# Kernel tuning notes

Measured on AMD Instinct MI355X. Metric: run time of the kernel, lower is better.

The kernel has to match this reference:

```python
import jax, jax.numpy as jnp
import numpy as np

B, CIN, COUT, H, W = 4, 256, 256, 96, 96
GN_GROUPS = 16
EPS = 1e-5


def setup_inputs() -> dict:
    key = jax.random.key(0)
    k0, k1, k2, k3 = jax.random.split(key, 4)
    x = jax.random.normal(k0, (B, CIN, H, W), jnp.float32)
    offset = jax.random.normal(k1, (B, 18, H, W), jnp.float32)
    mask = jax.random.uniform(k2, (B, 9, H, W), jnp.float32)  # modulation scalars (sigmoid-range)
    weight = jax.random.normal(k3, (COUT, CIN, 3, 3), jnp.float32) * 0.02
    gamma = jnp.ones((COUT,), jnp.float32)
    beta = jnp.zeros((COUT,), jnp.float32)
    return {"x": x, "offset": offset, "mask": mask, "weight": weight, "gamma": gamma, "beta": beta}


def _bilinear(xf, py, px, Hs, Ws):
    # xf: [B, C, H*W] flattened input; py/px: [B, H, W] sample coords -> [B, C, H, W]
    y0 = jnp.floor(py)
    x0 = jnp.floor(px)
    acc = jnp.zeros((xf.shape[0], xf.shape[1], py.shape[1], py.shape[2]), xf.dtype)
    for dy in (0, 1):
        for dx in (0, 1):
            yy = y0 + dy
            xx = x0 + dx
            wgt = (1.0 - jnp.abs(py - yy)) * (1.0 - jnp.abs(px - xx))
            valid = (yy >= 0) & (yy < Hs) & (xx >= 0) & (xx < Ws)  # zero-pad outside
            yi = jnp.clip(yy, 0, Hs - 1).astype(jnp.int32)
            xi = jnp.clip(xx, 0, Ws - 1).astype(jnp.int32)
            idx = (yi * Ws + xi).reshape(py.shape[0], -1)  # [B, H*W]
            g = jax.vmap(lambda xb, ib: xb[:, ib])(xf, idx)  # [B, C, H*W]
            g = g.reshape(acc.shape)
            acc = acc + g * (wgt * valid.astype(xf.dtype))[:, None]
    return acc


def _modulated_deform_conv(x, offset, mask, weight):
    # 3x3, stride=1, pad=1, dilation=1, deform_groups=1, no bias
    Bz, C, Hs, Ws = x.shape
    hh = jnp.arange(Hs, dtype=x.dtype)
    ww = jnp.arange(Ws, dtype=x.dtype)
    base_y, base_x = jnp.meshgrid(hh, ww, indexing="ij")  # [H, W]
    xf = x.reshape(Bz, C, Hs * Ws)
    out = jnp.zeros((Bz, weight.shape[0], Hs, Ws), x.dtype)
    for k in range(9):  # fixed 3x3 kernel taps
        ki, kj = k // 3, k % 3
        py = base_y[None] + (ki - 1) + offset[:, 2 * k]      # dy channel
        px = base_x[None] + (kj - 1) + offset[:, 2 * k + 1]  # dx channel
        val = _bilinear(xf, py, px, Hs, Ws) * mask[:, k][:, None]  # [B, CIN, H, W]
        out = out + jnp.einsum("oc,bchw->bohw", weight[:, :, ki, kj], val)
    return out


def _group_norm(x, gamma, beta):
    Bz, C, Hs, Ws = x.shape
    xr = x.reshape(Bz, GN_GROUPS, C // GN_GROUPS, Hs, Ws)
    mu = xr.mean(axis=(2, 3, 4), keepdims=True)
    var = xr.var(axis=(2, 3, 4), keepdims=True)
    xn = ((xr - mu) * jax.lax.rsqrt(var + EPS)).reshape(Bz, C, Hs, Ws)
    return xn * gamma[None, :, None, None] + beta[None, :, None, None]


def reference(x, offset, mask, weight, gamma, beta):
    y = _modulated_deform_conv(x, offset, mask, weight)
    return _group_norm(y, gamma, beta)
```

## Files before the change

### kernel.cpp

```cpp
#include <hip/hip_runtime.h>
#include <hip/hip_bf16.h>
#include <cstdint>

typedef short  short8  __attribute__((ext_vector_type(8)));
typedef ushort ushort8 __attribute__((ext_vector_type(8)));
typedef float  f32x4   __attribute__((ext_vector_type(4)));

#define BATCH 4
#define CIN   256
#define COUT  256
#define HH    96
#define WW    96
#define HWSZ  9216
#define GN_G  16
#define EPSV  1e-5f
#define BN    144
#define NPB   64
#define NWG   (BATCH*NPB)

__device__ __forceinline__ float bf2f(ushort u) {
    return __uint_as_float(((uint32_t)u) << 16);
}
__device__ __forceinline__ ushort f2bf(float f) {
    uint32_t u = __float_as_uint(f);
    u += 0x7FFFu + ((u >> 16) & 1u);
    return (ushort)(u >> 16);
}

__global__ __launch_bounds__(256)
void nhwc_kernel(const float* __restrict__ x, ushort* __restrict__ xn) {
    __shared__ ushort tile[64][66];
    const int b  = blockIdx.z;
    const int cb = blockIdx.y * 64;
    const int pb = blockIdx.x * 64;
    const int t  = threadIdx.x;
    {
        const int pl = t & 63;
        const int cq = t >> 6;
        #pragma unroll
        for (int i = 0; i < 16; ++i) {
            const int c = cq * 16 + i;
            tile[c][pl] = f2bf(x[((size_t)b * CIN + cb + c) * HWSZ + pb + pl]);
        }
    }
    __syncthreads();
    {
        const int cl = t & 63;
        const int pq = t >> 6;
        #pragma unroll
        for (int i = 0; i < 16; ++i) {
            const int p = pq * 16 + i;
            xn[((size_t)b * HWSZ + pb + p) * CIN + cb + cl] = tile[cl][p];
        }
    }
}

__global__ __launch_bounds__(256)
void repack_w_kernel(const float* __restrict__ w, ushort* __restrict__ wp) {
    const int d    = blockIdx.x * 256 + threadIdx.x;
    const int j    = d & 7;
    const int cout = (d >> 3) & 255;
    const int kb8  = d >> 11;
    const int ktap = kb8 >> 5;
    const int cin  = ((kb8 & 31) << 3) | j;
    wp[d] = f2bf(w[cout * (CIN * 9) + cin * 9 + ktap]);
}

__global__ __launch_bounds__(512, 2)
void dcn_mfma_kernel(const ushort* __restrict__ xn, const float* __restrict__ off,
                     const float* __restrict__ msk, const ushort* __restrict__ wp,
                     float* __restrict__ out, float* __restrict__ part) {
    __shared__ __align__(16) ushort buf[2][BN * 128];
    __shared__ int    s_idx[2][BN][4];
    __shared__ float  s_wgt[2][BN][4];

    const int bid  = blockIdx.x;
    const int swz  = (bid & 7) * (NWG / 8) + (bid >> 3);
    const int b    = swz / NPB;
    const int pblk = swz - b * NPB;
    const int p0   = pblk * BN;

    const int t    = threadIdx.x;
    const int lane = t & 63;
    const int wid  = t >> 6;
    const int cg   = wid & 3;
    const int kh   = wid >> 2;

    auto coords = [&](int k) {
        if (t < BN) {
            const int slot = k & 1;
            const int pos  = p0 + t;
            const int hh   = pos / WW;
            const int ww   = pos - hh * WW;
            const size_t obase = ((size_t)b * 18 + 2 * k) * HWSZ + pos;
            const float oy = off[obase];
            const float ox = off[obase + HWSZ];
            const float m  = msk[((size_t)b * 9 + k) * HWSZ + pos];
            const float py = (float)(hh + k / 3 - 1) + oy;
            const float px = (float)(ww + k % 3 - 1) + ox;
            const float y0 = floorf(py), x0 = floorf(px);
            #pragma unroll
            for (int dy = 0; dy < 2; ++dy)
                #pragma unroll
                for (int dx = 0; dx < 2; ++dx) {
                    const float yy = y0 + (float)dy, xx = x0 + (float)dx;
                    const float wb = (1.f - fabsf(py - yy)) * (1.f - fabsf(px - xx));
                    const bool valid = (yy >= 0.f) && (yy < (float)HH) && (xx >= 0.f) && (xx < (float)WW);
                    int yi = (int)yy; yi = yi < 0 ? 0 : (yi > HH - 1 ? HH - 1 : yi);
                    int xi = (int)xx; xi = xi < 0 ? 0 : (xi > WW - 1 ? WW - 1 : xi);
                    s_idx[slot][t][dy * 2 + dx] = yi * WW + xi;
                    s_wgt[slot][t][dy * 2 + dx] = valid ? wb * m : 0.f;
                }
        }
    };

    const int sp  = lane >> 4;
    const int c16 = lane & 15;
    auto stage = [&](int c, ushort* dstbuf) {
        const int tap  = c >> 1;
        const int half = c & 1;
        const int slot = tap & 1;
        const ushort* xb = xn + (size_t)b * HWSZ * CIN + half * 128 + c16 * 8;
        #pragma unroll
        for (int g = 0; g < 5; ++g) {
            const bool active = (g < 4) || (sp < 2);
            const int p = wid * 18 + ((g < 4) ? (g * 4 + sp) : (16 + sp));
            if (active) {
                float vacc[8] = {0.f, 0.f, 0.f, 0.f, 0.f, 0.f, 0.f, 0.f};
                #pragma unroll
                for (int cr = 0; cr < 4; ++cr) {
                    const int   ix = s_idx[slot][p][cr];
                    const float w  = s_wgt[slot][p][cr];
                    const ushort8 v = *(const ushort8*)(xb + (size_t)ix * CIN);
                    #pragma unroll
                    for (int j = 0; j < 8; ++j)
                        vacc[j] += w * bf2f(v[j]);
                }
                ushort8 o;
                #pragma unroll
                for (int j = 0; j < 8; j += 2) {
                    const __hip_bfloat162 h2 = __float22bfloat162_rn(float2{vacc[j], vacc[j + 1]});
                    const uint32_t u = *reinterpret_cast<const uint32_t*>(&h2);
                    o[j]     = (ushort)u;
                    o[j + 1] = (ushort)(u >> 16);
                }
                char* drow = (char*)dstbuf + p * 256;
                *(ushort8*)(drow + ((c16 * 16) ^ ((p & 15) << 4))) = o;
            }
        }
    };

    f32x4 acc[4][9];
    #pragma unroll
    for (int i = 0; i < 4; ++i)
        #pragma unroll
        for (int j = 0; j < 9; ++j)
            acc[i][j] = (f32x4){0.f, 0.f, 0.f, 0.f};

    const int arow = lane & 15;
    const int akb  = lane >> 4;

    auto loadA = [&](int kb8base, int ks, short8 af[4]) {
        const ushort* wrow = wp + ((size_t)(kb8base + ks * 4 + akb) * COUT + cg * 64 + arow) * 8;
        #pragma unroll
        for (int mt = 0; mt < 4; ++mt)
            af[mt] = *(const short8*)(wrow + mt * 16 * 8);
    };

    auto mfma_chunk = [&](int kb8base, const ushort* src, short8 afA[4]) {
        const char* srow = (const char*)src;
        short8 afB[4];
        #pragma unroll
        for (int ks = 0; ks < 2; ++ks) {
            const int ksg = kh * 2 + ks;
            if (ks == 0) loadA(kb8base, kh * 2 + 1, afB);
            short8* afc = ks ? afB : afA;
            #pragma unroll
            for (int nt = 0; nt < 9; ++nt) {
                const int row = arow + nt * 16;
                const short8 bfr = *(const short8*)(srow + row * 256 + ((ksg * 64 + akb * 16) ^ ((row & 15) << 4)));
                #pragma unroll
                for (int mt = 0; mt < 4; ++mt)
                    acc[mt][nt] = __builtin_amdgcn_mfma_f32_16x16x32_bf16(
                        afc[mt], bfr, acc[mt][nt], 0, 0, 0);
            }
        }
    };

    coords(0);
    __syncthreads();
    stage(0, buf[0]);
    __syncthreads();
    for (int c = 0; c < 18; ++c) {
        if (c < 17) stage(c + 1, buf[(c + 1) & 1]);
        if (!(c & 1) && (c >> 1) + 1 < 9) coords((c >> 1) + 1);
        short8 afA[4];
        loadA(c * 16, kh * 2, afA);
        mfma_chunk(c * 16, buf[c & 1], afA);
        __syncthreads();
    }

    {
        f32x4* s_xch = reinterpret_cast<f32x4*>(&buf[0][0]);
        const int plane = cg * 64 + lane;
        #pragma unroll
        for (int mt = 0; mt < 4; ++mt) {
            if (wid >= 4) {
                #pragma unroll
                for (int nt = 0; nt < 9; ++nt)
                    s_xch[plane * 10 + nt] = acc[mt][nt];
            }
            __syncthreads();
            if (wid < 4) {
                #pragma unroll
                for (int nt = 0; nt < 9; ++nt)
                    acc[mt][nt] += s_xch[plane * 10 + nt];
            }
            __syncthreads();
        }
    }

    if (wid < 4) {
        const int prow = lane & 15;
        const int crow = (lane >> 4) * 4;
        #pragma unroll
        for (int mt = 0; mt < 4; ++mt) {
            const int cout = cg * 64 + mt * 16 + crow;
            #pragma unroll
            for (int nt = 0; nt < 9; ++nt) {
                const int opos = p0 + nt * 16 + prow;
                float* op = out + ((size_t)b * COUT + cout) * HWSZ + opos;
                #pragma unroll
                for (int r = 0; r < 4; ++r)
                    op[(size_t)r * HWSZ] = acc[mt][nt][r];
            }
        }

        #pragma unroll
        for (int mt = 0; mt < 4; ++mt) {
            float s = 0.f, q = 0.f;
            #pragma unroll
            for (int nt = 0; nt < 9; ++nt)
                #pragma unroll
                for (int r = 0; r < 4; ++r) {
                    const float v = acc[mt][nt][r];
                    s += v; q += v * v;
                }
            #pragma unroll
            for (int o = 32; o > 0; o >>= 1) {
                s += __shfl_xor(s, o);
                q += __shfl_xor(q, o);
            }
            if (lane == 0) {
                const int bg = b * GN_G + cg * 4 + mt;
                part[((size_t)bg * NPB + pblk) * 2]     = s;
                part[((size_t)bg * NPB + pblk) * 2 + 1] = q;
            }
        }
    }
}

__global__ void gn_final_kernel(const float* __restrict__ part, float* __restrict__ stats) {
    const int t  = threadIdx.x;
    const int bg = t >> 2;
    const int j  = t & 3;
    float s = 0.f, q = 0.f;
    for (int i = j; i < NPB; i += 4) {
        s += part[((size_t)bg * NPB + i) * 2];
        q += part[((size_t)bg * NPB + i) * 2 + 1];
    }
    s += __shfl_xor(s, 1); q += __shfl_xor(q, 1);
    s += __shfl_xor(s, 2); q += __shfl_xor(q, 2);
    if (j == 0) {
        const float invn = 1.f / (float)((COUT / GN_G) * HWSZ);
        const float mean = s * invn;
        stats[bg * 2]     = mean;
        stats[bg * 2 + 1] = q * invn - mean * mean;
    }
}

__global__ __launch_bounds__(256)
void gn_apply_kernel(float* __restrict__ y, const float* __restrict__ stats,
                     const float* __restrict__ gamma, const float* __restrict__ beta) {
    const int i = blockIdx.x * 256 + threadIdx.x;
    const int e = i * 4;
    const int c  = (e / HWSZ) & (COUT - 1);
    const int bg = e / (HWSZ * (COUT / GN_G));
    const float mean = stats[bg * 2];
    const float var  = stats[bg * 2 + 1];
    const float inv  = rsqrtf(var + EPSV);
    const float sc = inv * gamma[c];
    const float sh = beta[c] - mean * sc;
    float4 v = ((float4*)y)[i];
    v.x = v.x * sc + sh;
    v.y = v.y * sc + sh;
    v.z = v.z * sc + sh;
    v.w = v.w * sc + sh;
    ((float4*)y)[i] = v;
}

extern "C" void kernel_launch(void* const* d_in, const int* in_sizes, int n_in,
                              void* d_out, int out_size, void* d_ws, size_t ws_size,
                              hipStream_t stream) {
    const float* x      = (const float*)d_in[0];
    const float* offset = (const float*)d_in[1];
    const float* mask   = (const float*)d_in[2];
    const float* weight = (const float*)d_in[3];
    const float* gamma  = (const float*)d_in[4];
    const float* beta   = (const float*)d_in[5];
    float* out = (float*)d_out;

    ushort* xn    = (ushort*)d_ws;
    ushort* wp    = xn + (size_t)BATCH * HWSZ * CIN;
    float*  part  = (float*)(wp + (size_t)9 * CIN * COUT);
    float*  stats = part + (size_t)BATCH * GN_G * NPB * 2;

    {
        dim3 g(HWSZ / 64, CIN / 64, BATCH);
        nhwc_kernel<<<g, 256, 0, stream>>>(x, xn);
    }
    repack_w_kernel<<<9 * CIN * COUT / 256, 256, 0, stream>>>(weight, wp);

    dcn_mfma_kernel<<<NWG, 512, 0, stream>>>(xn, offset, mask, wp, out, part);

    gn_final_kernel<<<1, 256, 0, stream>>>(part, stats);
    gn_apply_kernel<<<(size_t)BATCH * COUT * HWSZ / 4 / 256, 256, 0, stream>>>(out, stats, gamma, beta);
}
```

Baseline: 105.0 us.

## Use fp16 gather math, bf16 intermediate output, and fuse GN stats into apply

Stores the NHWC input as fp16 and does the bilinear gather blend with packed half-precision vector math instead of per-element fp32 accumulation. When the workspace is large enough, the conv writes its pre-norm output as bf16 to a scratch buffer, and the GroupNorm apply kernel reads that and writes fp32, roughly halving intermediate traffic. The separate GN statistics kernel is folded into the apply kernel, with each block reducing its group's partial sums, which removes one launch. This adds fp16 range and rounding risk in the sampling step and bf16 rounding of the pre-norm activations.

```diff
diff --git a/kernel.cpp b/kernel.cpp
--- a/kernel.cpp
+++ b/kernel.cpp
@@ -2,9 +2,10 @@
 #include <hip/hip_bf16.h>
 #include <cstdint>
 
-typedef short  short8  __attribute__((ext_vector_type(8)));
-typedef ushort ushort8 __attribute__((ext_vector_type(8)));
-typedef float  f32x4   __attribute__((ext_vector_type(4)));
+typedef short    short8  __attribute__((ext_vector_type(8)));
+typedef ushort   ushort8 __attribute__((ext_vector_type(8)));
+typedef float    f32x4   __attribute__((ext_vector_type(4)));
+typedef _Float16 half8   __attribute__((ext_vector_type(8)));
 
 #define BATCH 4
 #define CIN   256
@@ -28,8 +29,8 @@
 }
 
 __global__ __launch_bounds__(256)
-void nhwc_kernel(const float* __restrict__ x, ushort* __restrict__ xn) {
-    __shared__ ushort tile[64][66];
+void nhwc_kernel(const float* __restrict__ x, _Float16* __restrict__ xn) {
+    __shared__ _Float16 tile[64][66];
     const int b  = blockIdx.z;
     const int cb = blockIdx.y * 64;
     const int pb = blockIdx.x * 64;
@@ -40,7 +41,7 @@
         #pragma unroll
         for (int i = 0; i < 16; ++i) {
             const int c = cq * 16 + i;
-            tile[c][pl] = f2bf(x[((size_t)b * CIN + cb + c) * HWSZ + pb + pl]);
+            tile[c][pl] = (_Float16)x[((size_t)b * CIN + cb + c) * HWSZ + pb + pl];
         }
     }
     __syncthreads();
@@ -67,9 +68,10 @@
 }
 
 __global__ __launch_bounds__(512, 2)
-void dcn_mfma_kernel(const ushort* __restrict__ xn, const float* __restrict__ off,
+void dcn_mfma_kernel(const _Float16* __restrict__ xn, const float* __restrict__ off,
                      const float* __restrict__ msk, const ushort* __restrict__ wp,
-                     float* __restrict__ out, float* __restrict__ part) {
+                     float* __restrict__ out, ushort* __restrict__ yb, int use_bf16,
+                     float* __restrict__ part) {
     __shared__ __align__(16) ushort buf[2][BN * 128];
     __shared__ int    s_idx[2][BN][4];
     __shared__ float  s_wgt[2][BN][4];
@@ -83,7 +85,7 @@
     const int t    = threadIdx.x;
     const int lane = t & 63;
     const int wid  = t >> 6;
-    const int cg   = wid & 3;
+    const int cgp  = wid & 3;
     const int kh   = wid >> 2;
 
     auto coords = [&](int k) {
@@ -120,26 +122,26 @@
         const int tap  = c >> 1;
         const int half = c & 1;
         const int slot = tap & 1;
-        const ushort* xb = xn + (size_t)b * HWSZ * CIN + half * 128 + c16 * 8;
+        const _Float16* xb = xn + (size_t)b * HWSZ * CIN + half * 128 + c16 * 8;
         #pragma unroll
         for (int g = 0; g < 5; ++g) {
             const bool active = (g < 4) || (sp < 2);
             const int p = wid * 18 + ((g < 4) ? (g * 4 + sp) : (16 + sp));
             if (active) {
-                float vacc[8] = {0.f, 0.f, 0.f, 0.f, 0.f, 0.f, 0.f, 0.f};
-                #pragma unroll
-                for (int cr = 0; cr < 4; ++cr) {
-                    const int   ix = s_idx[slot][p][cr];
-                    const float w  = s_wgt[slot][p][cr];
-                    const ushort8 v = *(const ushort8*)(xb + (size_t)ix * CIN);
-                    #pragma unroll
-                    for (int j = 0; j < 8; ++j)
-                        vacc[j] += w * bf2f(v[j]);
-                }
+                const _Float16 w0 = (_Float16)s_wgt[slot][p][0];
+                const _Float16 w1 = (_Float16)s_wgt[slot][p][1];
+                const _Float16 w2 = (_Float16)s_wgt[slot][p][2];
+                const _Float16 w3 = (_Float16)s_wgt[slot][p][3];
+                const half8 v0 = *(const half8*)(xb + (size_t)s_idx[slot][p][0] * CIN);
+                const half8 v1 = *(const half8*)(xb + (size_t)s_idx[slot][p][1] * CIN);
+                const half8 v2 = *(const half8*)(xb + (size_t)s_idx[slot][p][2] * CIN);
+                const half8 v3 = *(const half8*)(xb + (size_t)s_idx[slot][p][3] * CIN);
+                const half8 h = v0 * w0 + v1 * w1 + v2 * w2 + v3 * w3;
                 ushort8 o;
                 #pragma unroll
                 for (int j = 0; j < 8; j += 2) {
-                    const __hip_bfloat162 h2 = __float22bfloat162_rn(float2{vacc[j], vacc[j + 1]});
+                    const __hip_bfloat162 h2 =
+                        __float22bfloat162_rn(float2{(float)h[j], (float)h[j + 1]});
                     const uint32_t u = *reinterpret_cast<const uint32_t*>(&h2);
                     o[j]     = (ushort)u;
                     o[j + 1] = (ushort)(u >> 16);
@@ -161,7 +163,7 @@
     const int akb  = lane >> 4;
 
     auto loadA = [&](int kb8base, int ks, short8 af[4]) {
-        const ushort* wrow = wp + ((size_t)(kb8base + ks * 4 + akb) * COUT + cg * 64 + arow) * 8;
+        const ushort* wrow = wp + ((size_t)(kb8base + ks * 4 + akb) * COUT + cgp * 64 + arow) * 8;
         #pragma unroll
         for (int mt = 0; mt < 4; ++mt)
             af[mt] = *(const short8*)(wrow + mt * 16 * 8);
@@ -202,7 +204,7 @@
 
     {
         f32x4* s_xch = reinterpret_cast<f32x4*>(&buf[0][0]);
-        const int plane = cg * 64 + lane;
+        const int plane = cgp * 64 + lane;
         #pragma unroll
         for (int mt = 0; mt < 4; ++mt) {
             if (wid >= 4) {
@@ -223,16 +225,31 @@
     if (wid < 4) {
         const int prow = lane & 15;
         const int crow = (lane >> 4) * 4;
-        #pragma unroll
-        for (int mt = 0; mt < 4; ++mt) {
-            const int cout = cg * 64 + mt * 16 + crow;
-            #pragma unroll
-            for (int nt = 0; nt < 9; ++nt) {
-                const int opos = p0 + nt * 16 + prow;
-                float* op = out + ((size_t)b * COUT + cout) * HWSZ + opos;
-                #pragma unroll
-                for (int r = 0; r < 4; ++r)
-                    op[(size_t)r * HWSZ] = acc[mt][nt][r];
+        if (use_bf16) {
+            #pragma unroll
+            for (int mt = 0; mt < 4; ++mt) {
+                const int cout = cgp * 64 + mt * 16 + crow;
+                #pragma unroll
+                for (int nt = 0; nt < 9; ++nt) {
+                    const int opos = p0 + nt * 16 + prow;
+                    ushort* op = yb + ((size_t)b * COUT + cout) * HWSZ + opos;
+                    #pragma unroll
+                    for (int r = 0; r < 4; ++r)
+                        op[(size_t)r * HWSZ] = f2bf(acc[mt][nt][r]);
+                }
+            }
+        } else {
+            #pragma unroll
+            for (int mt = 0; mt < 4; ++mt) {
+                const int cout = cgp * 64 + mt * 16 + crow;
+                #pragma unroll
+                for (int nt = 0; nt < 9; ++nt) {
+                    const int opos = p0 + nt * 16 + prow;
+                    float* op = out + ((size_t)b * COUT + cout) * HWSZ + opos;
+                    #pragma unroll
+                    for (int r = 0; r < 4; ++r)
+                        op[(size_t)r * HWSZ] = acc[mt][nt][r];
+                }
             }
         }
 
@@ -252,7 +269,7 @@
                 q += __shfl_xor(q, o);
             }
             if (lane == 0) {
-                const int bg = b * GN_G + cg * 4 + mt;
+                const int bg = b * GN_G + cgp * 4 + mt;
                 part[((size_t)bg * NPB + pblk) * 2]     = s;
                 part[((size_t)bg * NPB + pblk) * 2 + 1] = q;
             }
@@ -260,43 +277,85 @@
     }
 }
 
-__global__ void gn_final_kernel(const float* __restrict__ part, float* __restrict__ stats) {
+__global__ __launch_bounds__(256)
+void gn_apply_bf16_kernel(const ushort* __restrict__ yb, const float* __restrict__ part,
+                          const float* __restrict__ gamma, const float* __restrict__ beta,
+                          float* __restrict__ out) {
+    __shared__ float sm[2];
+    const int bg = blockIdx.y;
     const int t  = threadIdx.x;
-    const int bg = t >> 2;
-    const int j  = t & 3;
-    float s = 0.f, q = 0.f;
-    for (int i = j; i < NPB; i += 4) {
-        s += part[((size_t)bg * NPB + i) * 2];
-        q += part[((size_t)bg * NPB + i) * 2 + 1];
-    }
-    s += __shfl_xor(s, 1); q += __shfl_xor(q, 1);
-    s += __shfl_xor(s, 2); q += __shfl_xor(q, 2);
-    if (j == 0) {
-        const float invn = 1.f / (float)((COUT / GN_G) * HWSZ);
-        const float mean = s * invn;
-        stats[bg * 2]     = mean;
-        stats[bg * 2 + 1] = q * invn - mean * mean;
+    if (t < 64) {
+        float s = part[((size_t)bg * NPB + t) * 2];
+        float q = part[((size_t)bg * NPB + t) * 2 + 1];
+        #pragma unroll
+        for (int o = 32; o > 0; o >>= 1) {
+            s += __shfl_xor(s, o);
+            q += __shfl_xor(q, o);
+        }
+        if (t == 0) {
+            const float invn = 1.f / (float)((COUT / GN_G) * HWSZ);
+            const float mean = s * invn;
+            const float var  = q * invn - mean * mean;
+            sm[0] = mean;
+            sm[1] = rsqrtf(var + EPSV);
+        }
+    }
+    __syncthreads();
+    const float mean = sm[0], inv = sm[1];
+    const size_t base = (size_t)bg * (COUT / GN_G) * HWSZ + (size_t)blockIdx.x * 16384;
+    #pragma unroll 2
+    for (int it = 0; it < 8; ++it) {
+        const size_t e = base + ((size_t)(it * 256 + t)) * 8;
+        const int c = (int)((e / HWSZ) & (COUT - 1));
+        const float sc = inv * gamma[c];
+        const float sh = beta[c] - mean * sc;
+        const ushort8 v = *(const ushort8*)(yb + e);
+        float4 o0, o1;
+        o0.x = bf2f(v[0]) * sc + sh;  o0.y = bf2f(v[1]) * sc + sh;
+        o0.z = bf2f(v[2]) * sc + sh;  o0.w = bf2f(v[3]) * sc + sh;
+        o1.x = bf2f(v[4]) * sc + sh;  o1.y = bf2f(v[5]) * sc + sh;
+        o1.z = bf2f(v[6]) * sc + sh;  o1.w = bf2f(v[7]) * sc + sh;
+        *(float4*)(out + e)     = o0;
+        *(float4*)(out + e + 4) = o1;
     }
 }
 
 __global__ __launch_bounds__(256)
-void gn_apply_kernel(float* __restrict__ y, const float* __restrict__ stats,
-                     const float* __restrict__ gamma, const float* __restrict__ beta) {
-    const int i = blockIdx.x * 256 + threadIdx.x;
-    const int e = i * 4;
-    const int c  = (e / HWSZ) & (COUT - 1);
-    const int bg = e / (HWSZ * (COUT / GN_G));
-    const float mean = stats[bg * 2];
-    const float var  = stats[bg * 2 + 1];
-    const float inv  = rsqrtf(var + EPSV);
-    const float sc = inv * gamma[c];
-    const float sh = beta[c] - mean * sc;
-    float4 v = ((float4*)y)[i];
-    v.x = v.x * sc + sh;
-    v.y = v.y * sc + sh;
-    v.z = v.z * sc + sh;
-    v.w = v.w * sc + sh;
-    ((float4*)y)[i] = v;
+void gn_apply_f32_kernel(float* __restrict__ y, const float* __restrict__ part,
+                         const float* __restrict__ gamma, const float* __restrict__ beta) {
+    __shared__ float sm[2];
+    const int bg = blockIdx.y;
+    const int t  = threadIdx.x;
+    if (t < 64) {
+        float s = part[((size_t)bg * NPB + t) * 2];
+        float q = part[((size_t)bg * NPB + t) * 2 + 1];
+        #pragma unroll
+        for (int o = 32; o > 0; o >>= 1) {
+            s += __shfl_xor(s, o);
+            q += __shfl_xor(q, o);
+        }
+        if (t == 0) {
+            const float invn = 1.f / (float)((COUT / GN_G) * HWSZ);
+            const float mean = s * invn;
+            const float var  = q * invn - mean * mean;
+            sm[0] = mean;
+            sm[1] = rsqrtf(var + EPSV);
+        }
+    }
+    __syncthreads();
+    const float mean = sm[0], inv = sm[1];
+    const size_t base = (size_t)bg * (COUT / GN_G) * HWSZ + (size_t)blockIdx.x * 16384;
+    #pragma unroll 2
+    for (int it = 0; it < 16; ++it) {
+        const size_t e = base + ((size_t)(it * 256 + t)) * 4;
+        const int c = (int)((e / HWSZ) & (COUT - 1));
+        const float sc = inv * gamma[c];
+        const float sh = beta[c] - mean * sc;
+        float4 v = *(float4*)(y + e);
+        v.x = v.x * sc + sh;  v.y = v.y * sc + sh;
+        v.z = v.z * sc + sh;  v.w = v.w * sc + sh;
+        *(float4*)(y + e) = v;
+    }
 }
 
 extern "C" void kernel_launch(void* const* d_in, const int* in_sizes, int n_in,
@@ -310,10 +369,15 @@
     const float* beta   = (const float*)d_in[5];
     float* out = (float*)d_out;
 
-    ushort* xn    = (ushort*)d_ws;
-    ushort* wp    = xn + (size_t)BATCH * HWSZ * CIN;
-    float*  part  = (float*)(wp + (size_t)9 * CIN * COUT);
-    float*  stats = part + (size_t)BATCH * GN_G * NPB * 2;
+    const size_t XN = (size_t)BATCH * HWSZ * CIN;
+    const size_t WP = (size_t)9 * CIN * COUT;
+    const size_t PT = (size_t)BATCH * GN_G * NPB * 2;
+    _Float16* xn   = (_Float16*)d_ws;
+    ushort*   wp   = (ushort*)d_ws + XN;
+    float*    part = (float*)((ushort*)d_ws + XN + WP);
+    ushort*   yb   = (ushort*)(part + PT);
+    const size_t need = (XN + WP) * 2 + PT * 4 + (size_t)BATCH * COUT * HWSZ * 2;
+    const int use_bf16 = (ws_size >= need) ? 1 : 0;
 
     {
         dim3 g(HWSZ / 64, CIN / 64, BATCH);
@@ -321,8 +385,11 @@
     }
     repack_w_kernel<<<9 * CIN * COUT / 256, 256, 0, stream>>>(weight, wp);
 
-    dcn_mfma_kernel<<<NWG, 512, 0, stream>>>(xn, offset, mask, wp, out, part);
-
-    gn_final_kernel<<<1, 256, 0, stream>>>(part, stats);
-    gn_apply_kernel<<<(size_t)BATCH * COUT * HWSZ / 4 / 256, 256, 0, stream>>>(out, stats, gamma, beta);
-}
+    dcn_mfma_kernel<<<NWG, 512, 0, stream>>>(xn, offset, mask, wp, out, yb, use_bf16, part);
+
+    dim3 gg(9, BATCH * GN_G);
+    if (use_bf16)
+        gn_apply_bf16_kernel<<<gg, 256, 0, stream>>>(yb, part, gamma, beta, out);
+    else
+        gn_apply_f32_kernel<<<gg, 256, 0, stream>>>(out, part, gamma, beta);
+}
```

Result: faster. 95.50 us (-9.0%).
